# Performance work log

Measured on AMD Instinct MI355X. Metric: run time of the kernel, lower is better.

The kernel has to match this reference:

```python
import jax, jax.numpy as jnp
import numpy as np

B = 4096          # sum(hierchy_struc) time series
L = 32            # number of hierarchy levels = len(hierchy_struc)
D = 512           # d_model
DQK = 512         # d_model_qk
DV = 512          # d_model_v
H = 8             # heads
HIER = [128] * 32 # hierchy_struc
GROUP = np.repeat(np.arange(L), HIER)  # group id of each batch row, shape [B]


def setup_inputs() -> dict:
    key = jax.random.key(0)
    ks = jax.random.split(key, 9)
    s_in = 1.0 / np.sqrt(D)
    s_v = 1.0 / np.sqrt(DV)
    return {
        "x": jax.random.normal(ks[0], (B, L, D), jnp.float32),
        "Wq": jax.random.normal(ks[1], (D, DQK), jnp.float32) * s_in,
        "bq": jax.random.normal(ks[2], (DQK,), jnp.float32) * s_in,
        "Wk": jax.random.normal(ks[3], (D, DQK), jnp.float32) * s_in,
        "bk": jax.random.normal(ks[4], (DQK,), jnp.float32) * s_in,
        "Wv": jax.random.normal(ks[5], (D, DV), jnp.float32) * s_in,
        "bv": jax.random.normal(ks[6], (DV,), jnp.float32) * s_in,
        "Wo": jax.random.normal(ks[7], (DV, DV), jnp.float32) * s_v,
        "bo": jax.random.normal(ks[8], (DV,), jnp.float32) * s_v,
    }


def reference(x, Wq, bq, Wk, bk, Wv, bv, Wo, bo):
    # QKV projections -> (B, H, L, dh)
    def split_heads(y):
        b, l, d = y.shape
        return y.reshape(b, l, H, d // H).transpose(0, 2, 1, 3)

    q = split_heads(x @ Wq + bq)
    k = split_heads(x @ Wk + bk)
    v = split_heads(x @ Wv + bv)

    dh = q.shape[-1]
    scores = jnp.einsum("bhqd,bhkd->bhqk", q, k) / float(np.sqrt(dh))
    p_attn = jax.nn.softmax(scores, axis=-1)  # (B, H, L, L)

    # hierarchical post-softmax mask: batch row b only keeps query row GROUP[b]
    group = jnp.asarray(GROUP)
    row_keep = (jnp.arange(L)[None, :] == group[:, None]).astype(p_attn.dtype)
    p_attn = p_attn * row_keep[:, None, :, None]

    ctx = jnp.einsum("bhqk,bhkd->bhqd", p_attn, v)          # (B, H, L, dh)
    ctx = ctx.transpose(0, 2, 1, 3).reshape(B, L, DV)        # merge heads

    # p_attn.sum(dim=2) -> (B,H,L); transpose(1,2) -> (B,L,H); mean(dim=2) -> (B,L)
    p_attn_sum = p_attn.sum(axis=2).mean(axis=1)

    out = ctx @ Wo + bo
    return out, p_attn_sum
```

## Files before the change

kernel.cpp:

```cpp
#include <hip/hip_runtime.h>
#include <hip/hip_bf16.h>
#include <math.h>

typedef unsigned short u16;
typedef __attribute__((ext_vector_type(4))) float f32x4;
typedef __attribute__((ext_vector_type(4))) unsigned short u16x4;
typedef __attribute__((ext_vector_type(8))) short s16x8;
typedef __attribute__((ext_vector_type(4))) unsigned int u32x4;

__device__ __forceinline__ u16 f2bf(float f) {
  union { float f; unsigned int u; } v; v.f = f;
  unsigned int r = v.u + 0x7FFFu + ((v.u >> 16) & 1u);
  return (u16)(r >> 16);
}
__device__ __forceinline__ float bf2f(u16 u) {
  union { unsigned int u; float f; } v; v.u = ((unsigned int)u) << 16;
  return v.f;
}
__device__ __forceinline__ void gload16(const void* g, void* l) {
  __builtin_amdgcn_global_load_lds(
      (const __attribute__((address_space(1))) unsigned int*)g,
      (__attribute__((address_space(3))) unsigned int*)l, 16, 0, 0);
}

__global__ __launch_bounds__(256)
void prep_kernel(const float* __restrict__ x,
                 const float* __restrict__ Wq, const float* __restrict__ Wv,
                 const float* __restrict__ Wo, const float* __restrict__ Wk,
                 u16* __restrict__ wqT, u16* __restrict__ wvT,
                 u16* __restrict__ woT, u16* __restrict__ wkB,
                 u16* __restrict__ xg)
{
  const int blk = blockIdx.x;
  const int t = threadIdx.x;
  if (blk < 192) {
    __shared__ u16 tile[64 * 72];
    int m = blk >> 6, tno = blk & 63;
    const float* W = (m == 0) ? Wq : (m == 1) ? Wv : Wo;
    u16* WT = (m == 0) ? wqT : (m == 1) ? wvT : woT;
    int r0 = (tno >> 3) * 64, c0 = (tno & 7) * 64;
    int tr = t >> 4;
    int tc = (t & 15) * 4;
#pragma unroll
    for (int ii = 0; ii < 4; ii++) {
      int r = tr + ii * 16;
      f32x4 v = *(const f32x4*)(W + (long)(r0 + r) * 512 + c0 + tc);
#pragma unroll
      for (int j = 0; j < 4; j++) tile[(tc + j) * 72 + r] = f2bf(v[j]);
    }
    __syncthreads();
#pragma unroll
    for (int ii = 0; ii < 4; ii++) {
      int r = tr + ii * 16;
      u16x4 o;
#pragma unroll
      for (int j = 0; j < 4; j++) o[j] = tile[r * 72 + tc + j];
      *(u16x4*)(WT + (long)(c0 + r) * 512 + r0 + tc) = o;
    }
  } else if (blk < 448) {
    int i = (blk - 192) * 256 + t;
    f32x4 v = *(const f32x4*)(Wk + (long)i * 4);
    u16x4 o;
#pragma unroll
    for (int j = 0; j < 4; j++) o[j] = f2bf(v[j]);
    *(u16x4*)(wkB + (long)i * 4) = o;
  } else {
    int i = (blk - 448) * 256 + t;
    int bb = i >> 7, d = (i & 127) * 4;
    int g = bb >> 7;
    f32x4 v = *(const f32x4*)(x + ((long)bb * 32 + g) * 512 + d);
    u16x4 o;
#pragma unroll
    for (int j = 0; j < 4; j++) o[j] = f2bf(v[j]);
    *(u16x4*)(xg + (long)bb * 512 + d) = o;
  }
}

template<int BM, int BN, bool OUT_BF16, bool CROW_REMAP, bool ADD_BIAS>
__global__ __launch_bounds__(256)
void gemm_tn(const u16* __restrict__ A, int lda, long aZ,
             const u16* __restrict__ B, int ldb, long bZ,
             void* __restrict__ Cv, int ldc, long cZ,
             const float* __restrict__ bias, int biasZ, int K)
{
  constexpr int BK = 64;
  constexpr int CS = BN + 8;
  constexpr int STG = BM * BK + BN * BK;
  constexpr int SMEM = (STG > BM * CS) ? STG : BM * CS;
  __shared__ u16 smem[SMEM];
  u16* As = smem;
  u16* Bs = smem + BM * BK;
  const int z = blockIdx.z;
  const u16* Ab = A + (long)z * aZ + (long)blockIdx.y * BM * lda;
  const u16* Bb = B + (long)z * bZ + (long)blockIdx.x * BN * ldb;
  const int tid = threadIdx.x;
  const int wave = tid >> 6, lane = tid & 63;
  constexpr int WM = BM / 2, WN = BN / 2;
  const int wm = wave >> 1, wn = wave & 1;
  constexpr int MF = WM / 16, NF = WN / 16;
  constexpr int ACH = (BM * BK * 2) / 1024;
  constexpr int BCH = (BN * BK * 2) / 1024;
  f32x4 acc[MF][NF] = {};
  const int rIn  = lane >> 3;
  const int cOff = (lane & 7) * 8;

  for (int kb = 0; kb < K; kb += BK) {
#pragma unroll
    for (int ch = 0; ch < ACH / 4; ch++) {
      int c = wave + ch * 4;
      int r = c * 8 + rIn;
      gload16(Ab + (long)r * lda + kb + cOff, As + c * 512 + lane * 8);
    }
#pragma unroll
    for (int ch = 0; ch < BCH / 4; ch++) {
      int c = wave + ch * 4;
      int r = c * 8 + rIn;
      gload16(Bb + (long)r * ldb + kb + cOff, Bs + c * 512 + lane * 8);
    }
    __syncthreads();
#pragma unroll
    for (int ks = 0; ks < BK; ks += 32) {
      s16x8 af[MF], bfv[NF];
#pragma unroll
      for (int i = 0; i < MF; i++)
        af[i] = *(const s16x8*)(As + (wm * WM + i * 16 + (lane & 15)) * BK + ks + ((lane >> 4) * 8));
#pragma unroll
      for (int j = 0; j < NF; j++)
        bfv[j] = *(const s16x8*)(Bs + (wn * WN + j * 16 + (lane & 15)) * BK + ks + ((lane >> 4) * 8));
#pragma unroll
      for (int i = 0; i < MF; i++)
#pragma unroll
        for (int j = 0; j < NF; j++)
          acc[i][j] = __builtin_amdgcn_mfma_f32_16x16x32_bf16(af[i], bfv[j], acc[i][j], 0, 0, 0);
    }
    __syncthreads();
  }

  const long cz = (long)z * cZ;
  if constexpr (OUT_BF16) {
#pragma unroll
    for (int j = 0; j < NF; j++) {
      int colL = wn * WN + j * 16 + (lane & 15);
      float bvv = 0.f;
      if (ADD_BIAS) bvv = bias[(long)z * biasZ + blockIdx.x * BN + colL];
#pragma unroll
      for (int i = 0; i < MF; i++) {
#pragma unroll
        for (int r4 = 0; r4 < 4; r4++) {
          int rowL = wm * WM + i * 16 + ((lane >> 4) << 2) + r4;
          smem[rowL * CS + colL] = f2bf(acc[i][j][r4] + bvv);
        }
      }
    }
    __syncthreads();
    constexpr int CPR = BN / 8;
    constexpr int CHUNKS = BM * CPR;
    u16* Cb = (u16*)Cv + cz + (long)blockIdx.y * BM * ldc + blockIdx.x * BN;
#pragma unroll 4
    for (int c = tid; c < CHUNKS; c += 256) {
      int row = c / CPR, co = (c % CPR) * 8;
      s16x8 vv = *(const s16x8*)(smem + row * CS + co);
      *(s16x8*)(Cb + (long)row * ldc + co) = vv;
    }
  } else {
    const int colBase = blockIdx.x * BN + wn * WN;
    const int rowBase = blockIdx.y * BM + wm * WM;
#pragma unroll
    for (int j = 0; j < NF; j++) {
      int col = colBase + j * 16 + (lane & 15);
      float bvv = 0.f;
      if (ADD_BIAS) bvv = bias[(long)z * biasZ + col];
#pragma unroll
      for (int i = 0; i < MF; i++) {
#pragma unroll
        for (int r4 = 0; r4 < 4; r4++) {
          int row = rowBase + i * 16 + ((lane >> 4) << 2) + r4;
          float v = acc[i][j][r4] + bvv;
          if constexpr (CROW_REMAP) {
            ((float*)Cv)[((long)row * 32 + (row >> 7)) * ldc + col] = v;
          } else {
            ((float*)Cv)[cz + (long)row * ldc + col] = v;
          }
        }
      }
    }
  }
}

#define PSUM_OFF 67108864L

__global__ __launch_bounds__(256)
void attn_kernel(const float* __restrict__ x, u16* __restrict__ QKY,
                 const float* __restrict__ bo, float* __restrict__ out)
{
  const int b = blockIdx.x;
  const int t = threadIdx.x;
  const int wave = t >> 6, lane = t & 63;
  __shared__ u16 xs[16384];
  __shared__ float scl[32 * 8];
  __shared__ float pl[8 * 32];

  const f32x4* x4 = (const f32x4*)(x + (long)b * 16384);
  {
    const f32x4* bo4 = (const f32x4*)bo;
    f32x4* ob = (f32x4*)(out + (long)b * 16384);
#pragma unroll
    for (int it = 0; it < 16; ++it) {
      int i = t + it * 256;
      __builtin_nontemporal_store(bo4[i & 127], &ob[i]);
    }
  }
#pragma unroll
  for (int it = 0; it < 16; ++it) {
    int i = t + it * 256;
    int l = (i & 3) * 8 + (i >> 9);
    int dq = (i >> 2) & 127;
    f32x4 v = __builtin_nontemporal_load(&x4[l * 128 + dq]);
    u16x4 uv;
    uv[0] = f2bf(v[0]); uv[1] = f2bf(v[1]); uv[2] = f2bf(v[2]); uv[3] = f2bf(v[3]);
    int S = ((l >> 2) << 5) + (dq >> 2);
    int off = (S << 6) + ((l & 3) << 4) + ((((dq & 3) << 2)) ^ ((S & 1) << 3));
    *(u16x4*)(xs + off) = uv;
  }
  __syncthreads();

  if (wave < 2) {
    const int l0 = wave * 16;
    const int arow = l0 + (lane & 15);
    const int brow = lane & 15;
    const u16* qkg = QKY + (long)b * 4096;
    f32x4 acc = {0.f, 0.f, 0.f, 0.f};
#pragma unroll
    for (int ks = 0; ks < 16; ks++) {
      int d0 = ks * 32 + (lane >> 4) * 8;
      int S = ((arow >> 2) << 5) + (d0 >> 4);
      int aoff = (S << 6) + ((arow & 3) << 4) + ((d0 & 15) ^ ((S & 1) << 3));
      s16x8 af = *(const s16x8*)(xs + aoff);
      s16x8 bf = *(const s16x8*)(qkg + brow * 512 + d0);
      acc = __builtin_amdgcn_mfma_f32_16x16x32_bf16(af, bf, acc, 0, 0, 0);
    }
    if (brow < 8) {
#pragma unroll
      for (int r = 0; r < 4; r++)
        scl[(l0 + (lane >> 4) * 4 + r) * 8 + brow] = acc[r] * 0.125f;
    }
  }
  __syncthreads();

  const int h = t >> 5, l = t & 31;
  {
    float s = scl[l * 8 + h];
    float m = s;
#pragma unroll
    for (int mk = 16; mk; mk >>= 1) m = fmaxf(m, __shfl_xor(m, mk, 32));
    float ex = expf(s - m);
    float sum = ex;
#pragma unroll
    for (int mk = 16; mk; mk >>= 1) sum += __shfl_xor(sum, mk, 32);
    pl[h * 32 + l] = ex / sum;
  }
  __syncthreads();
  if (t < 32) {
    float ps = 0.f;
#pragma unroll
    for (int hh = 0; hh < 8; hh++) ps += pl[hh * 32 + t];
    out[PSUM_OFF + (long)b * 32 + t] = ps * 0.125f;
  }
  float a0[8] = {}, a1[8] = {};
  const int dbase = (t & 31) * 16;
  const int stag = (t >> 2) & 3;
#pragma unroll 4
  for (int i2 = 0; i2 < 32; i2++) {
    int ll = (i2 + stag) & 31;
    float pv = pl[h * 32 + ll];
    int S0 = ((ll >> 2) << 5) + (t & 31);
    int base = (S0 << 6) + ((ll & 3) << 4);
    int sw = (S0 & 1) << 3;
    s16x8 xa = *(const s16x8*)(xs + base + sw);
    s16x8 xc = *(const s16x8*)(xs + base + (8 ^ sw));
#pragma unroll
    for (int e = 0; e < 8; e++) {
      a0[e] += pv * bf2f((u16)xa[e]);
      a1[e] += pv * bf2f((u16)xc[e]);
    }
  }
  u16* yrow = QKY + (long)b * 4096 + h * 512 + dbase;
  s16x8 o0, o1;
#pragma unroll
  for (int e = 0; e < 8; e++) { o0[e] = (short)f2bf(a0[e]); o1[e] = (short)f2bf(a1[e]); }
  *(s16x8*)(yrow) = o0;
  *(s16x8*)(yrow + 8) = o1;
}

extern "C" void kernel_launch(void* const* d_in, const int* in_sizes, int n_in,
                              void* d_out, int out_size, void* d_ws, size_t ws_size,
                              hipStream_t stream)
{
  const float* x  = (const float*)d_in[0];
  const float* Wq = (const float*)d_in[1];
  const float* bq = (const float*)d_in[2];
  const float* Wk = (const float*)d_in[3];
  const float* Wv = (const float*)d_in[5];
  const float* bv = (const float*)d_in[6];
  const float* Wo = (const float*)d_in[7];
  const float* bo = (const float*)d_in[8];
  float* out = (float*)d_out;

  char* w = (char*)d_ws;
  u16* wqT = (u16*)(w);
  u16* wkB = (u16*)(w + 524288);
  u16* wvT = (u16*)(w + 1048576);
  u16* woT = (u16*)(w + 1572864);
  u16* xg  = (u16*)(w + 2097152);
  u16* qbf = (u16*)(w + 6291456);
  u16* qky = (u16*)(w + 10485760);
  u16* ctx = (u16*)(w + 44040192);

  prep_kernel<<<2496, 256, 0, stream>>>(x, Wq, Wv, Wo, Wk, wqT, wvT, woT, wkB, xg);
  gemm_tn<64, 64, true, false, true><<<dim3(8, 64, 1), 256, 0, stream>>>(
      xg, 512, 0, wqT, 512, 0, qbf, 512, 0, bq, 0, 512);
  gemm_tn<128, 128, true, false, false><<<dim3(4, 32, 8), 256, 0, stream>>>(
      qbf, 512, 64, wkB, 512, 64, qky, 4096, 512, nullptr, 0, 64);
  attn_kernel<<<4096, 256, 0, stream>>>(x, qky, bo, out);
  gemm_tn<64, 64, true, false, true><<<dim3(1, 64, 8), 256, 0, stream>>>(
      qky, 4096, 512, wvT, 512, 32768, ctx, 512, 64, bv, 64, 512);
  gemm_tn<64, 64, false, true, true><<<dim3(8, 64, 1), 256, 0, stream>>>(
      ctx, 512, 0, woT, 512, 0, out, 512, 0, bo, 0, 512);
}
```

Before: 159.6 us.

## Process two batch rows per attention block with register-prefetched x loads

The attention kernel now handles two batch rows per block, halving the grid. While the first row is being computed, the x tile for the second row is loaded into registers, so global load latency overlaps with compute. The cost is 64 extra VGPRs for the prefetch buffer, which may reduce occupancy, and half as many blocks to spread across CUs.

```diff
diff --git a/kernel.cpp b/kernel.cpp
--- a/kernel.cpp
+++ b/kernel.cpp
@@ -193,103 +193,129 @@
 void attn_kernel(const float* __restrict__ x, u16* __restrict__ QKY,
                  const float* __restrict__ bo, float* __restrict__ out)
 {
-  const int b = blockIdx.x;
   const int t = threadIdx.x;
   const int wave = t >> 6, lane = t & 63;
   __shared__ u16 xs[16384];
   __shared__ float scl[32 * 8];
   __shared__ float pl[8 * 32];
 
-  const f32x4* x4 = (const f32x4*)(x + (long)b * 16384);
-  {
-    const f32x4* bo4 = (const f32x4*)bo;
-    f32x4* ob = (f32x4*)(out + (long)b * 16384);
-#pragma unroll
-    for (int it = 0; it < 16; ++it) {
-      int i = t + it * 256;
-      __builtin_nontemporal_store(bo4[i & 127], &ob[i]);
-    }
-  }
+  int lidx[16], didx[16];
 #pragma unroll
   for (int it = 0; it < 16; ++it) {
     int i = t + it * 256;
-    int l = (i & 3) * 8 + (i >> 9);
-    int dq = (i >> 2) & 127;
-    f32x4 v = __builtin_nontemporal_load(&x4[l * 128 + dq]);
-    u16x4 uv;
-    uv[0] = f2bf(v[0]); uv[1] = f2bf(v[1]); uv[2] = f2bf(v[2]); uv[3] = f2bf(v[3]);
-    int S = ((l >> 2) << 5) + (dq >> 2);
-    int off = (S << 6) + ((l & 3) << 4) + ((((dq & 3) << 2)) ^ ((S & 1) << 3));
-    *(u16x4*)(xs + off) = uv;
-  }
-  __syncthreads();
-
-  if (wave < 2) {
-    const int l0 = wave * 16;
-    const int arow = l0 + (lane & 15);
-    const int brow = lane & 15;
-    const u16* qkg = QKY + (long)b * 4096;
-    f32x4 acc = {0.f, 0.f, 0.f, 0.f};
-#pragma unroll
-    for (int ks = 0; ks < 16; ks++) {
-      int d0 = ks * 32 + (lane >> 4) * 8;
-      int S = ((arow >> 2) << 5) + (d0 >> 4);
-      int aoff = (S << 6) + ((arow & 3) << 4) + ((d0 & 15) ^ ((S & 1) << 3));
-      s16x8 af = *(const s16x8*)(xs + aoff);
-      s16x8 bf = *(const s16x8*)(qkg + brow * 512 + d0);
-      acc = __builtin_amdgcn_mfma_f32_16x16x32_bf16(af, bf, acc, 0, 0, 0);
-    }
-    if (brow < 8) {
-#pragma unroll
-      for (int r = 0; r < 4; r++)
-        scl[(l0 + (lane >> 4) * 4 + r) * 8 + brow] = acc[r] * 0.125f;
-    }
-  }
-  __syncthreads();
-
-  const int h = t >> 5, l = t & 31;
+    lidx[it] = (i & 3) * 8 + (i >> 9);
+    didx[it] = (i >> 2) & 127;
+  }
+
+  f32x4 vbuf[16];
   {
-    float s = scl[l * 8 + h];
-    float m = s;
-#pragma unroll
-    for (int mk = 16; mk; mk >>= 1) m = fmaxf(m, __shfl_xor(m, mk, 32));
-    float ex = expf(s - m);
-    float sum = ex;
-#pragma unroll
-    for (int mk = 16; mk; mk >>= 1) sum += __shfl_xor(sum, mk, 32);
-    pl[h * 32 + l] = ex / sum;
-  }
-  __syncthreads();
-  if (t < 32) {
-    float ps = 0.f;
-#pragma unroll
-    for (int hh = 0; hh < 8; hh++) ps += pl[hh * 32 + t];
-    out[PSUM_OFF + (long)b * 32 + t] = ps * 0.125f;
-  }
-  float a0[8] = {}, a1[8] = {};
-  const int dbase = (t & 31) * 16;
-  const int stag = (t >> 2) & 3;
+    const f32x4* x4 = (const f32x4*)(x + (long)(blockIdx.x * 2) * 16384);
+#pragma unroll
+    for (int it = 0; it < 16; ++it)
+      vbuf[it] = __builtin_nontemporal_load(&x4[lidx[it] * 128 + didx[it]]);
+  }
+
+  for (int sub = 0; sub < 2; ++sub) {
+    const int b = blockIdx.x * 2 + sub;
+
+#pragma unroll
+    for (int it = 0; it < 16; ++it) {
+      int l = lidx[it], dq = didx[it];
+      f32x4 v = vbuf[it];
+      u16x4 uv;
+      uv[0] = f2bf(v[0]); uv[1] = f2bf(v[1]); uv[2] = f2bf(v[2]); uv[3] = f2bf(v[3]);
+      int S = ((l >> 2) << 5) + (dq >> 2);
+      int off = (S << 6) + ((l & 3) << 4) + ((((dq & 3) << 2)) ^ ((S & 1) << 3));
+      *(u16x4*)(xs + off) = uv;
+    }
+    __syncthreads();
+
+    if (sub == 0) {
+      const f32x4* x4n = (const f32x4*)(x + (long)(b + 1) * 16384);
+#pragma unroll
+      for (int it = 0; it < 16; ++it)
+        vbuf[it] = __builtin_nontemporal_load(&x4n[lidx[it] * 128 + didx[it]]);
+    }
+
+    {
+      const f32x4* bo4 = (const f32x4*)bo;
+      f32x4* ob = (f32x4*)(out + (long)b * 16384);
+#pragma unroll
+      for (int it = 0; it < 16; ++it) {
+        int i = t + it * 256;
+        __builtin_nontemporal_store(bo4[i & 127], &ob[i]);
+      }
+    }
+
+    if (wave < 2) {
+      const int l0 = wave * 16;
+      const int arow = l0 + (lane & 15);
+      const int brow = lane & 15;
+      const u16* qkg = QKY + (long)b * 4096;
+      f32x4 acc = {0.f, 0.f, 0.f, 0.f};
+#pragma unroll
+      for (int ks = 0; ks < 16; ks++) {
+        int d0 = ks * 32 + (lane >> 4) * 8;
+        int S = ((arow >> 2) << 5) + (d0 >> 4);
+        int aoff = (S << 6) + ((arow & 3) << 4) + ((d0 & 15) ^ ((S & 1) << 3));
+        s16x8 af = *(const s16x8*)(xs + aoff);
+        s16x8 bf = *(const s16x8*)(qkg + brow * 512 + d0);
+        acc = __builtin_amdgcn_mfma_f32_16x16x32_bf16(af, bf, acc, 0, 0, 0);
+      }
+      if (brow < 8) {
+#pragma unroll
+        for (int r = 0; r < 4; r++)
+          scl[(l0 + (lane >> 4) * 4 + r) * 8 + brow] = acc[r] * 0.125f;
+      }
+    }
+    __syncthreads();
+
+    const int h = t >> 5, l = t & 31;
+    {
+      float s = scl[l * 8 + h];
+      float m = s;
+#pragma unroll
+      for (int mk = 16; mk; mk >>= 1) m = fmaxf(m, __shfl_xor(m, mk, 32));
+      float ex = expf(s - m);
+      float sum = ex;
+#pragma unroll
+      for (int mk = 16; mk; mk >>= 1) sum += __shfl_xor(sum, mk, 32);
+      pl[h * 32 + l] = ex / sum;
+    }
+    __syncthreads();
+    if (t < 32) {
+      float ps = 0.f;
+#pragma unroll
+      for (int hh = 0; hh < 8; hh++) ps += pl[hh * 32 + t];
+      out[PSUM_OFF + (long)b * 32 + t] = ps * 0.125f;
+    }
+    float a0[8] = {}, a1[8] = {};
+    const int dbase = (t & 31) * 16;
+    const int stag = (t >> 2) & 3;
 #pragma unroll 4
-  for (int i2 = 0; i2 < 32; i2++) {
-    int ll = (i2 + stag) & 31;
-    float pv = pl[h * 32 + ll];
-    int S0 = ((ll >> 2) << 5) + (t & 31);
-    int base = (S0 << 6) + ((ll & 3) << 4);
-    int sw = (S0 & 1) << 3;
-    s16x8 xa = *(const s16x8*)(xs + base + sw);
-    s16x8 xc = *(const s16x8*)(xs + base + (8 ^ sw));
-#pragma unroll
-    for (int e = 0; e < 8; e++) {
-      a0[e] += pv * bf2f((u16)xa[e]);
-      a1[e] += pv * bf2f((u16)xc[e]);
-    }
-  }
-  u16* yrow = QKY + (long)b * 4096 + h * 512 + dbase;
-  s16x8 o0, o1;
-#pragma unroll
-  for (int e = 0; e < 8; e++) { o0[e] = (short)f2bf(a0[e]); o1[e] = (short)f2bf(a1[e]); }
-  *(s16x8*)(yrow) = o0;
-  *(s16x8*)(yrow + 8) = o1;
+    for (int i2 = 0; i2 < 32; i2++) {
+      int ll = (i2 + stag) & 31;
+      float pv = pl[h * 32 + ll];
+      int S0 = ((ll >> 2) << 5) + (t & 31);
+      int base = (S0 << 6) + ((ll & 3) << 4);
+      int sw = (S0 & 1) << 3;
+      s16x8 xa = *(const s16x8*)(xs + base + sw);
+      s16x8 xc = *(const s16x8*)(xs + base + (8 ^ sw));
+#pragma unroll
+      for (int e = 0; e < 8; e++) {
+        a0[e] += pv * bf2f((u16)xa[e]);
+        a1[e] += pv * bf2f((u16)xc[e]);
+      }
+    }
+    u16* yrow = QKY + (long)b * 4096 + h * 512 + dbase;
+    s16x8 o0, o1;
+#pragma unroll
+    for (int e = 0; e < 8; e++) { o0[e] = (short)f2bf(a0[e]); o1[e] = (short)f2bf(a1[e]); }
+    *(s16x8*)(yrow) = o0;
+    *(s16x8*)(yrow + 8) = o1;
+
+    __syncthreads();
+  }
 }
 
 extern "C" void kernel_launch(void* const* d_in, const int* in_sizes, int n_in,
@@ -321,7 +347,7 @@
       xg, 512, 0, wqT, 512, 0, qbf, 512, 0, bq, 0, 512);
   gemm_tn<128, 128, true, false, false><<<dim3(4, 32, 8), 256, 0, stream>>>(
       qbf, 512, 64, wkB, 512, 64, qky, 4096, 512, nullptr, 0, 64);
-  attn_kernel<<<4096, 256, 0, stream>>>(x, qky, bo, out);
+  attn_kernel<<<2048, 256, 0, stream>>>(x, qky, bo, out);
   gemm_tn<64, 64, true, false, true><<<dim3(1, 64, 8), 256, 0, stream>>>(
       qky, 4096, 512, wvT, 512, 32768, ctx, 512, 64, bv, 64, 512);
   gemm_tn<64, 64, false, true, true><<<dim3(8, 64, 1), 256, 0, stream>>>(
```

Result: slower. 165.8 us (+3.9%).
